# Kernel optimization log

Hardware: AMD Instinct MI355X
Metric: run time of the kernel (lower is better)

## Reference

```python
import jax, jax.numpy as jnp
import numpy as np

TEMPERATURE = 0.5
NEG_FILL = -9000000000000000.0


def setup_inputs() -> dict:
    key = jax.random.key(0)
    k1, k2 = jax.random.split(key)
    z1 = jax.random.normal(k1, (4096, 256), dtype=jnp.float32)
    z2 = jax.random.normal(k2, (4096, 256), dtype=jnp.float32)
    return {"z1": z1, "z2": z2}


def reference(z1, z2):
    N = z1.shape[0]
    z = jnp.concatenate([z1, z2], axis=0)  # [2N, d]
    # cosine similarity: normalize once (eps matches torch's 1e-8) then GEMM
    norm = jnp.maximum(jnp.linalg.norm(z, axis=-1, keepdims=True), 1e-8)
    zn = z / norm
    sim = (zn @ zn.T) / TEMPERATURE  # [2N, 2N]
    # mask out self-similarity on the diagonal
    diag = jnp.eye(2 * N, dtype=bool)
    sim = jnp.where(diag, NEG_FILL, sim)
    labels = jnp.concatenate([jnp.arange(N) + N, jnp.arange(N)])  # positive pairs
    logp = jax.nn.log_softmax(sim, axis=-1)
    loss = -jnp.mean(jnp.take_along_axis(logp, labels[:, None], axis=1))
    return loss
```

## Files before the change

kernel.cpp:

```cpp
#include <hip/hip_runtime.h>
#include <hip/hip_bf16.h>


#define TWO_N 8192
#define NPAIR 4096
#define DDIM  256
#define NT    64
#define NBLK  (NT * (NT + 1) / 2)
#define INV_T 2.0f
#define GEMM_GRID 256

typedef __attribute__((ext_vector_type(8))) short bf16x8;
typedef __attribute__((ext_vector_type(4))) float f32x4;

typedef __attribute__((address_space(1))) void gvoid_t;
typedef __attribute__((address_space(3))) void lvoid_t;

__device__ __forceinline__ void gload_lds16(const void* g, void* l) {
    __builtin_amdgcn_global_load_lds((gvoid_t*)g, (lvoid_t*)l, 16, 0, 0);
}

__global__ void k_normalize(const float* __restrict__ z1,
                            const float* __restrict__ z2,
                            __hip_bfloat16* __restrict__ zn,
                            float* __restrict__ e_diag,
                            float* __restrict__ pos,
                            float* __restrict__ row_sumexp,
                            float* __restrict__ out) {
    if (threadIdx.x < 8) row_sumexp[blockIdx.x * 8 + threadIdx.x] = 0.0f;
    if (blockIdx.x == 0 && threadIdx.x == 0) out[0] = 0.0f;

    const int w    = threadIdx.x >> 6;
    const int lane = threadIdx.x & 63;
    const int i    = blockIdx.x * 4 + w;

    float4 a = ((const float4*)(z1 + (size_t)i * DDIM))[lane];
    float4 b = ((const float4*)(z2 + (size_t)i * DDIM))[lane];

    float s1 = a.x * a.x + a.y * a.y + a.z * a.z + a.w * a.w;
    float s2 = b.x * b.x + b.y * b.y + b.z * b.z + b.w * b.w;
    float dd = a.x * b.x + a.y * b.y + a.z * b.z + a.w * b.w;
#pragma unroll
    for (int m = 1; m < 64; m <<= 1) {
        s1 += __shfl_xor(s1, m, 64);
        s2 += __shfl_xor(s2, m, 64);
        dd += __shfl_xor(dd, m, 64);
    }

    float inv1 = 1.0f / fmaxf(sqrtf(s1), 1e-8f);
    float inv2 = 1.0f / fmaxf(sqrtf(s2), 1e-8f);

    __hip_bfloat16 q1[4], q2[4];
    q1[0] = __float2bfloat16(a.x * inv1); q1[1] = __float2bfloat16(a.y * inv1);
    q1[2] = __float2bfloat16(a.z * inv1); q1[3] = __float2bfloat16(a.w * inv1);
    q2[0] = __float2bfloat16(b.x * inv2); q2[1] = __float2bfloat16(b.y * inv2);
    q2[2] = __float2bfloat16(b.z * inv2); q2[3] = __float2bfloat16(b.w * inv2);

    float qs1 = 0.0f, qs2 = 0.0f;
#pragma unroll
    for (int j = 0; j < 4; ++j) {
        float f1 = __bfloat162float(q1[j]);
        float f2 = __bfloat162float(q2[j]);
        qs1 += f1 * f1;
        qs2 += f2 * f2;
    }
#pragma unroll
    for (int m = 1; m < 64; m <<= 1) {
        qs1 += __shfl_xor(qs1, m, 64);
        qs2 += __shfl_xor(qs2, m, 64);
    }

    *reinterpret_cast<uint2*>(zn + (size_t)i * DDIM + lane * 4) =
        *reinterpret_cast<uint2*>(q1);
    *reinterpret_cast<uint2*>(zn + (size_t)(i + NPAIR) * DDIM + lane * 4) =
        *reinterpret_cast<uint2*>(q2);

    if (lane == 0) {
        e_diag[i]         = __expf(qs1 * INV_T);
        e_diag[i + NPAIR] = __expf(qs2 * INV_T);
        pos[i]            = dd * inv1 * inv2 * INV_T;
    }
}

__global__ __launch_bounds__(512, 2)
void k_gemm_sumexp(const __hip_bfloat16* __restrict__ zn,
                   float* __restrict__ row_sumexp) {
    __shared__ __align__(128) __hip_bfloat16 Asmem[128 * DDIM];

    const int tid  = threadIdx.x;
    const int lane = tid & 63;
    const int w    = tid >> 6;
    const int wr   = w >> 2;
    const int wc   = w & 3;
    const int lr   = lane & 15;
    const int quad = lane >> 4;

    const int t0 = (blockIdx.x * NBLK) >> 8;
    const int t1 = ((blockIdx.x + 1) * NBLK) >> 8;

    int b = t0;
    int rt = (int)(64.5f - sqrtf(64.5f * 64.5f - 2.0f * (float)b));
    if (rt < 0) rt = 0;
    if (rt > NT - 1) rt = NT - 1;
    while (rt > 0 && NT * rt - (rt * (rt - 1)) / 2 > b) --rt;
    while (NT * (rt + 1) - ((rt + 1) * rt) / 2 <= b) ++rt;
    int ct = rt + (b - (NT * rt - (rt * (rt - 1)) / 2));

    int cur_rt = -1;
    f32x4 acc[4][2];
    int  pRow = 0, pCol = 0;
    bool pDiag = false, havePrev = false;

    auto epilogue = [&]() {
        float rs[4][4], cs[2];
#pragma unroll
        for (int mi = 0; mi < 4; ++mi)
#pragma unroll
            for (int r = 0; r < 4; ++r) rs[mi][r] = 0.0f;
        cs[0] = cs[1] = 0.0f;
#pragma unroll
        for (int mi = 0; mi < 4; ++mi)
#pragma unroll
            for (int ni = 0; ni < 2; ++ni)
#pragma unroll
                for (int r = 0; r < 4; ++r) {
                    float e = __expf(acc[mi][ni][r] * INV_T);
                    rs[mi][r] += e;
                    cs[ni] += e;
                }
#pragma unroll
        for (int mi = 0; mi < 4; ++mi)
#pragma unroll
            for (int r = 0; r < 4; ++r) {
                float v = rs[mi][r];
                v += __shfl_xor(v, 1, 64);
                v += __shfl_xor(v, 2, 64);
                v += __shfl_xor(v, 4, 64);
                v += __shfl_xor(v, 8, 64);
                if (lr == 0)
                    atomicAdd(&row_sumexp[pRow + wr * 64 + mi * 16 + quad * 4 + r], v);
            }
        if (!pDiag) {
#pragma unroll
            for (int ni = 0; ni < 2; ++ni) {
                float v = cs[ni];
                v += __shfl_xor(v, 16, 64);
                v += __shfl_xor(v, 32, 64);
                if (quad == 0)
                    atomicAdd(&row_sumexp[pCol + wc * 32 + ni * 16 + lr], v);
            }
        }
    };

    for (int t = t0; t < t1; ++t) {
        const int  row_base = rt * 128;
        const int  col_base = ct * 128;
        const bool diag     = (rt == ct);
        const bool restage  = (rt != cur_rt);

        if (restage) {
            __syncthreads();
            const int ck = (tid & 24) | ((tid & 7) ^ ((tid >> 5) & 7));
            const char* gA = (const char*)(zn + (size_t)row_base * DDIM)
                           + (tid >> 5) * (DDIM * 2) + ck * 16;
            char* lA = (char*)Asmem + tid * 16;
#pragma unroll
            for (int j = 0; j < 8; ++j)
                gload_lds16(gA + (size_t)j * 16 * (DDIM * 2), lA + j * 8192);
            cur_rt = rt;
        }

        const __hip_bfloat16* gB0 =
            zn + (size_t)(col_base + wc * 32 + lr) * DDIM + quad * 8;
        bf16x8 Bfr[8][2];
#pragma unroll
        for (int ks = 0; ks < 8; ++ks) {
            const __hip_bfloat16* p0 = gB0 + ks * 32;
            const __hip_bfloat16* p1 = p0 + 16 * DDIM;
            asm volatile("global_load_dwordx4 %0, %1, off"
                         : "=v"(Bfr[ks][0]) : "v"(p0) : "memory");
            asm volatile("global_load_dwordx4 %0, %1, off"
                         : "=v"(Bfr[ks][1]) : "v"(p1) : "memory");
        }

        if (havePrev) epilogue();
        havePrev = true; pRow = row_base; pCol = col_base; pDiag = diag;

        int pa[4];
#pragma unroll
        for (int mi = 0; mi < 4; ++mi)
            pa[mi] = (wr * 64 + mi * 16 + lr) * (DDIM * 2) + ((quad ^ (lr & 7)) << 4);

        bf16x8 afc[4];
        if (restage) {
            asm volatile("s_waitcnt vmcnt(0)" ::: "memory");
            __syncthreads();
#pragma unroll
            for (int mi = 0; mi < 4; ++mi)
                afc[mi] = *(const bf16x8*)((const char*)Asmem + pa[mi]);
        } else {
#pragma unroll
            for (int mi = 0; mi < 4; ++mi)
                afc[mi] = *(const bf16x8*)((const char*)Asmem + pa[mi]);
            asm volatile("s_waitcnt vmcnt(16)" ::: "memory");
        }
        __builtin_amdgcn_sched_barrier(0);

#pragma unroll
        for (int mi = 0; mi < 4; ++mi)
#pragma unroll
            for (int ni = 0; ni < 2; ++ni)
                acc[mi][ni] = (f32x4){0.f, 0.f, 0.f, 0.f};

#pragma unroll
        for (int kstep = 0; kstep < 8; ++kstep) {
            bf16x8 afn[4];
            if (kstep < 7) {
                const int kn   = kstep + 1;
                const int koff = (kn >> 1) << 7;
                const int kx   = (kn & 1) << 6;
#pragma unroll
                for (int mi = 0; mi < 4; ++mi)
                    afn[mi] = *(const bf16x8*)((const char*)Asmem + ((pa[mi] ^ kx) + koff));
            }
#pragma unroll
            for (int mi = 0; mi < 4; ++mi)
#pragma unroll
                for (int ni = 0; ni < 2; ++ni)
                    acc[mi][ni] = __builtin_amdgcn_mfma_f32_16x16x32_bf16(
                        afc[mi], Bfr[kstep][ni], acc[mi][ni], 0, 0, 0);
            if (kstep < 7) {
#pragma unroll
                for (int mi = 0; mi < 4; ++mi) afc[mi] = afn[mi];
            }
        }

        if (++ct >= NT) { ++rt; ct = rt; }
    }

    epilogue();
}

__global__ void k_final(const float* __restrict__ row_sumexp,
                        const float* __restrict__ e_diag,
                        const float* __restrict__ pos,
                        float* __restrict__ out) {
    const int i    = blockIdx.x * 256 + threadIdx.x;
    const int w    = threadIdx.x >> 6;
    const int lane = threadIdx.x & 63;

    float t = logf(row_sumexp[i] - e_diag[i])
            + logf(row_sumexp[i + NPAIR] - e_diag[i + NPAIR])
            - 2.0f * pos[i];
#pragma unroll
    for (int m = 1; m < 64; m <<= 1) t += __shfl_xor(t, m, 64);

    __shared__ float ps[4];
    if (lane == 0) ps[w] = t;
    __syncthreads();
    if (threadIdx.x == 0) {
        float s = (ps[0] + ps[1] + ps[2] + ps[3]) * (1.0f / (float)TWO_N);
        atomicAdd(out, s);
    }
}

extern "C" void kernel_launch(void* const* d_in, const int* in_sizes, int n_in,
                              void* d_out, int out_size, void* d_ws, size_t ws_size,
                              hipStream_t stream) {
    const float* z1 = (const float*)d_in[0];
    const float* z2 = (const float*)d_in[1];
    float* out = (float*)d_out;

    char* ws = (char*)d_ws;
    __hip_bfloat16* zn  = (__hip_bfloat16*)ws;
    float* row_sumexp   = (float*)(ws + (size_t)TWO_N * DDIM * 2);
    float* e_diag       = row_sumexp + TWO_N;
    float* pos          = e_diag + TWO_N;

    k_normalize<<<NPAIR / 4, 256, 0, stream>>>(z1, z2, zn, e_diag, pos,
                                               row_sumexp, out);
    k_gemm_sumexp<<<GEMM_GRID, 512, 0, stream>>>(zn, row_sumexp);
    k_final<<<NPAIR / 256, 256, 0, stream>>>(row_sumexp, e_diag, pos, out);
}
```

Baseline: 128.6 us.

## Double GEMM grid, keep row sums in registers, split B loads around epilogue

Doubles the GEMM grid so each block handles about half as many triangular tiles. Row partial sums now stay in registers across all tiles that share a row tile, and the atomics are flushed only when the row tile changes, which cuts row atomics. B-fragment loads are split into two halves around the exp-accumulate epilogue so more of the global load latency is hidden. The risks are extra register pressure from the persistent row sums, and the `vmcnt(2)` wait, which lets the last B loads still be in flight when the first k-steps run.

```diff
diff --git a/kernel.cpp b/kernel.cpp
--- a/kernel.cpp
+++ b/kernel.cpp
@@ -8,7 +8,7 @@
 #define NT    64
 #define NBLK  (NT * (NT + 1) / 2)
 #define INV_T 2.0f
-#define GEMM_GRID 256
+#define GEMM_GRID 512
 
 typedef __attribute__((ext_vector_type(8))) short bf16x8;
 typedef __attribute__((ext_vector_type(4))) float f32x4;
@@ -95,8 +95,8 @@
     const int lr   = lane & 15;
     const int quad = lane >> 4;
 
-    const int t0 = (blockIdx.x * NBLK) >> 8;
-    const int t1 = ((blockIdx.x + 1) * NBLK) >> 8;
+    const int t0 = (int)(((long)blockIdx.x * NBLK) >> 9);
+    const int t1 = (int)(((long)(blockIdx.x + 1) * NBLK) >> 9);
 
     int b = t0;
     int rt = (int)(64.5f - sqrtf(64.5f * 64.5f - 2.0f * (float)b));
@@ -106,28 +106,43 @@
     while (NT * (rt + 1) - ((rt + 1) * rt) / 2 <= b) ++rt;
     int ct = rt + (b - (NT * rt - (rt * (rt - 1)) / 2));
 
+    int pa[4];
+#pragma unroll
+    for (int mi = 0; mi < 4; ++mi)
+        pa[mi] = (wr * 64 + mi * 16 + lr) * (DDIM * 2) + ((quad ^ (lr & 7)) << 4);
+
     int cur_rt = -1;
     f32x4 acc[4][2];
-    int  pRow = 0, pCol = 0;
+    float rs[4][4];
+#pragma unroll
+    for (int mi = 0; mi < 4; ++mi)
+#pragma unroll
+        for (int r = 0; r < 4; ++r) rs[mi][r] = 0.0f;
+    int  pCol = 0;
     bool pDiag = false, havePrev = false;
 
-    auto epilogue = [&]() {
-        float rs[4][4], cs[2];
+    auto epi_accum = [&](float& cs0, float& cs1) {
 #pragma unroll
         for (int mi = 0; mi < 4; ++mi)
 #pragma unroll
-            for (int r = 0; r < 4; ++r) rs[mi][r] = 0.0f;
-        cs[0] = cs[1] = 0.0f;
-#pragma unroll
-        for (int mi = 0; mi < 4; ++mi)
-#pragma unroll
-            for (int ni = 0; ni < 2; ++ni)
-#pragma unroll
-                for (int r = 0; r < 4; ++r) {
-                    float e = __expf(acc[mi][ni][r] * INV_T);
-                    rs[mi][r] += e;
-                    cs[ni] += e;
-                }
+            for (int r = 0; r < 4; ++r) {
+                float e0 = __expf(acc[mi][0][r] * INV_T);
+                float e1 = __expf(acc[mi][1][r] * INV_T);
+                rs[mi][r] += e0 + e1;
+                cs0 += e0;
+                cs1 += e1;
+            }
+    };
+    auto epi_cols = [&](float cs0, float cs1) {
+        if (pDiag) { cs0 = 0.0f; cs1 = 0.0f; }
+        cs0 += __shfl_xor(cs0, 16, 64); cs0 += __shfl_xor(cs0, 32, 64);
+        cs1 += __shfl_xor(cs1, 16, 64); cs1 += __shfl_xor(cs1, 32, 64);
+        if (quad == 0) {
+            atomicAdd(&row_sumexp[pCol + wc * 32 + lr], cs0);
+            atomicAdd(&row_sumexp[pCol + wc * 32 + 16 + lr], cs1);
+        }
+    };
+    auto flush_rows = [&](int rowb) {
 #pragma unroll
         for (int mi = 0; mi < 4; ++mi)
 #pragma unroll
@@ -138,18 +153,9 @@
                 v += __shfl_xor(v, 4, 64);
                 v += __shfl_xor(v, 8, 64);
                 if (lr == 0)
-                    atomicAdd(&row_sumexp[pRow + wr * 64 + mi * 16 + quad * 4 + r], v);
-            }
-        if (!pDiag) {
-#pragma unroll
-            for (int ni = 0; ni < 2; ++ni) {
-                float v = cs[ni];
-                v += __shfl_xor(v, 16, 64);
-                v += __shfl_xor(v, 32, 64);
-                if (quad == 0)
-                    atomicAdd(&row_sumexp[pCol + wc * 32 + ni * 16 + lr], v);
-            }
-        }
+                    atomicAdd(&row_sumexp[rowb + wr * 64 + mi * 16 + quad * 4 + r], v);
+                rs[mi][r] = 0.0f;
+            }
     };
 
     for (int t = t0; t < t1; ++t) {
@@ -158,7 +164,13 @@
         const bool diag     = (rt == ct);
         const bool restage  = (rt != cur_rt);
 
+        const __hip_bfloat16* gB0 =
+            zn + (size_t)(col_base + wc * 32 + lr) * DDIM + quad * 8;
+        bf16x8 Bfr[8][2];
+
         if (restage) {
+            if (havePrev) { float c0 = 0.f, c1 = 0.f; epi_accum(c0, c1); epi_cols(c0, c1); }
+            if (cur_rt >= 0) flush_rows(cur_rt * 128);
             __syncthreads();
             const int ck = (tid & 24) | ((tid & 7) ^ ((tid >> 5) & 7));
             const char* gA = (const char*)(zn + (size_t)row_base * DDIM)
@@ -167,50 +179,56 @@
 #pragma unroll
             for (int j = 0; j < 8; ++j)
                 gload_lds16(gA + (size_t)j * 16 * (DDIM * 2), lA + j * 8192);
+#pragma unroll
+            for (int ks = 0; ks < 8; ++ks) {
+                const __hip_bfloat16* p0 = gB0 + ks * 32;
+                const __hip_bfloat16* p1 = p0 + 16 * DDIM;
+                asm volatile("global_load_dwordx4 %0, %1, off"
+                             : "=v"(Bfr[ks][0]) : "v"(p0) : "memory");
+                asm volatile("global_load_dwordx4 %0, %1, off"
+                             : "=v"(Bfr[ks][1]) : "v"(p1) : "memory");
+            }
             cur_rt = rt;
-        }
-
-        const __hip_bfloat16* gB0 =
-            zn + (size_t)(col_base + wc * 32 + lr) * DDIM + quad * 8;
-        bf16x8 Bfr[8][2];
-#pragma unroll
-        for (int ks = 0; ks < 8; ++ks) {
-            const __hip_bfloat16* p0 = gB0 + ks * 32;
-            const __hip_bfloat16* p1 = p0 + 16 * DDIM;
-            asm volatile("global_load_dwordx4 %0, %1, off"
-                         : "=v"(Bfr[ks][0]) : "v"(p0) : "memory");
-            asm volatile("global_load_dwordx4 %0, %1, off"
-                         : "=v"(Bfr[ks][1]) : "v"(p1) : "memory");
-        }
-
-        if (havePrev) epilogue();
-        havePrev = true; pRow = row_base; pCol = col_base; pDiag = diag;
-
-        int pa[4];
-#pragma unroll
-        for (int mi = 0; mi < 4; ++mi)
-            pa[mi] = (wr * 64 + mi * 16 + lr) * (DDIM * 2) + ((quad ^ (lr & 7)) << 4);
-
-        bf16x8 afc[4];
-        if (restage) {
             asm volatile("s_waitcnt vmcnt(0)" ::: "memory");
             __syncthreads();
-#pragma unroll
-            for (int mi = 0; mi < 4; ++mi)
-                afc[mi] = *(const bf16x8*)((const char*)Asmem + pa[mi]);
         } else {
 #pragma unroll
-            for (int mi = 0; mi < 4; ++mi)
-                afc[mi] = *(const bf16x8*)((const char*)Asmem + pa[mi]);
-            asm volatile("s_waitcnt vmcnt(16)" ::: "memory");
+            for (int ks = 0; ks < 4; ++ks) {
+                const __hip_bfloat16* p0 = gB0 + ks * 32;
+                const __hip_bfloat16* p1 = p0 + 16 * DDIM;
+                asm volatile("global_load_dwordx4 %0, %1, off"
+                             : "=v"(Bfr[ks][0]) : "v"(p0) : "memory");
+                asm volatile("global_load_dwordx4 %0, %1, off"
+                             : "=v"(Bfr[ks][1]) : "v"(p1) : "memory");
+            }
+            float c0 = 0.f, c1 = 0.f;
+            epi_accum(c0, c1);
+#pragma unroll
+            for (int ks = 4; ks < 8; ++ks) {
+                const __hip_bfloat16* p0 = gB0 + ks * 32;
+                const __hip_bfloat16* p1 = p0 + 16 * DDIM;
+                asm volatile("global_load_dwordx4 %0, %1, off"
+                             : "=v"(Bfr[ks][0]) : "v"(p0) : "memory");
+                asm volatile("global_load_dwordx4 %0, %1, off"
+                             : "=v"(Bfr[ks][1]) : "v"(p1) : "memory");
+            }
+            epi_cols(c0, c1);
+            asm volatile("s_waitcnt vmcnt(2)" ::: "memory");
         }
         __builtin_amdgcn_sched_barrier(0);
 
+        pCol = col_base; pDiag = diag; havePrev = true;
+
 #pragma unroll
         for (int mi = 0; mi < 4; ++mi)
 #pragma unroll
             for (int ni = 0; ni < 2; ++ni)
                 acc[mi][ni] = (f32x4){0.f, 0.f, 0.f, 0.f};
+
+        bf16x8 afc[4];
+#pragma unroll
+        for (int mi = 0; mi < 4; ++mi)
+            afc[mi] = *(const bf16x8*)((const char*)Asmem + pa[mi]);
 
 #pragma unroll
         for (int kstep = 0; kstep < 8; ++kstep) {
@@ -238,7 +256,8 @@
         if (++ct >= NT) { ++rt; ct = rt; }
     }
 
-    epilogue();
+    { float c0 = 0.f, c1 = 0.f; epi_accum(c0, c1); epi_cols(c0, c1); }
+    flush_rows(cur_rt * 128);
 }
 
 __global__ void k_final(const float* __restrict__ row_sumexp,
```

Result: slower. 132.0 us (+2.6%).

## Replace symmetric triangular tiling with full row-panel GEMM and row-only sumexp

Applied to the files above, without the earlier changes.

Each block now owns one 128-row panel and an eighth of the columns, computing the full similarity matrix rather than only the upper triangle. Row sums accumulate in registers across tiles, with one set of atomics at the end and no column-sum atomics. This removes the triangular index setup, panel restaging and column atomic traffic. The cost is roughly double the matrix-multiply and exp work, plus a full memory wait each tile instead of a partial one.

```diff
diff --git a/kernel.cpp b/kernel.cpp
--- a/kernel.cpp
+++ b/kernel.cpp
@@ -6,9 +6,7 @@
 #define NPAIR 4096
 #define DDIM  256
 #define NT    64
-#define NBLK  (NT * (NT + 1) / 2)
 #define INV_T 2.0f
-#define GEMM_GRID 256
 
 typedef __attribute__((ext_vector_type(8))) short bf16x8;
 typedef __attribute__((ext_vector_type(4))) float f32x4;
@@ -83,8 +81,8 @@
 }
 
 __global__ __launch_bounds__(512, 2)
-void k_gemm_sumexp(const __hip_bfloat16* __restrict__ zn,
-                   float* __restrict__ row_sumexp) {
+void k_gemm_rows(const __hip_bfloat16* __restrict__ zn,
+                 float* __restrict__ row_sumexp) {
     __shared__ __align__(128) __hip_bfloat16 Asmem[128 * DDIM];
 
     const int tid  = threadIdx.x;
@@ -95,83 +93,48 @@
     const int lr   = lane & 15;
     const int quad = lane >> 4;
 
-    const int t0 = (blockIdx.x * NBLK) >> 8;
-    const int t1 = ((blockIdx.x + 1) * NBLK) >> 8;
-
-    int b = t0;
-    int rt = (int)(64.5f - sqrtf(64.5f * 64.5f - 2.0f * (float)b));
-    if (rt < 0) rt = 0;
-    if (rt > NT - 1) rt = NT - 1;
-    while (rt > 0 && NT * rt - (rt * (rt - 1)) / 2 > b) --rt;
-    while (NT * (rt + 1) - ((rt + 1) * rt) / 2 <= b) ++rt;
-    int ct = rt + (b - (NT * rt - (rt * (rt - 1)) / 2));
-
-    int cur_rt = -1;
+    const int panel    = blockIdx.x >> 3;
+    const int chunk    = blockIdx.x & 7;
+    const int row_base = panel * 128;
+
+    {
+        const int ck = (tid & 24) | ((tid & 7) ^ ((tid >> 5) & 7));
+        const char* gA = (const char*)(zn + (size_t)row_base * DDIM)
+                       + (tid >> 5) * (DDIM * 2) + ck * 16;
+        char* lA = (char*)Asmem + tid * 16;
+#pragma unroll
+        for (int j = 0; j < 8; ++j)
+            gload_lds16(gA + (size_t)j * 16 * (DDIM * 2), lA + j * 8192);
+    }
+
+    int pa[4];
+#pragma unroll
+    for (int mi = 0; mi < 4; ++mi)
+        pa[mi] = (wr * 64 + mi * 16 + lr) * (DDIM * 2) + ((quad ^ (lr & 7)) << 4);
+
     f32x4 acc[4][2];
-    int  pRow = 0, pCol = 0;
-    bool pDiag = false, havePrev = false;
-
-    auto epilogue = [&]() {
-        float rs[4][4], cs[2];
+    float rs[4][4];
+#pragma unroll
+    for (int mi = 0; mi < 4; ++mi)
+#pragma unroll
+        for (int r = 0; r < 4; ++r) rs[mi][r] = 0.0f;
+
+    auto epi_accum = [&]() {
 #pragma unroll
         for (int mi = 0; mi < 4; ++mi)
 #pragma unroll
-            for (int r = 0; r < 4; ++r) rs[mi][r] = 0.0f;
-        cs[0] = cs[1] = 0.0f;
-#pragma unroll
-        for (int mi = 0; mi < 4; ++mi)
-#pragma unroll
-            for (int ni = 0; ni < 2; ++ni)
-#pragma unroll
-                for (int r = 0; r < 4; ++r) {
-                    float e = __expf(acc[mi][ni][r] * INV_T);
-                    rs[mi][r] += e;
-                    cs[ni] += e;
-                }
-#pragma unroll
-        for (int mi = 0; mi < 4; ++mi)
-#pragma unroll
             for (int r = 0; r < 4; ++r) {
-                float v = rs[mi][r];
-                v += __shfl_xor(v, 1, 64);
-                v += __shfl_xor(v, 2, 64);
-                v += __shfl_xor(v, 4, 64);
-                v += __shfl_xor(v, 8, 64);
-                if (lr == 0)
-                    atomicAdd(&row_sumexp[pRow + wr * 64 + mi * 16 + quad * 4 + r], v);
+                rs[mi][r] += __expf(acc[mi][0][r] * INV_T)
+                           + __expf(acc[mi][1][r] * INV_T);
             }
-        if (!pDiag) {
-#pragma unroll
-            for (int ni = 0; ni < 2; ++ni) {
-                float v = cs[ni];
-                v += __shfl_xor(v, 16, 64);
-                v += __shfl_xor(v, 32, 64);
-                if (quad == 0)
-                    atomicAdd(&row_sumexp[pCol + wc * 32 + ni * 16 + lr], v);
-            }
-        }
     };
 
-    for (int t = t0; t < t1; ++t) {
-        const int  row_base = rt * 128;
-        const int  col_base = ct * 128;
-        const bool diag     = (rt == ct);
-        const bool restage  = (rt != cur_rt);
-
-        if (restage) {
-            __syncthreads();
-            const int ck = (tid & 24) | ((tid & 7) ^ ((tid >> 5) & 7));
-            const char* gA = (const char*)(zn + (size_t)row_base * DDIM)
-                           + (tid >> 5) * (DDIM * 2) + ck * 16;
-            char* lA = (char*)Asmem + tid * 16;
-#pragma unroll
-            for (int j = 0; j < 8; ++j)
-                gload_lds16(gA + (size_t)j * 16 * (DDIM * 2), lA + j * 8192);
-            cur_rt = rt;
-        }
-
+#pragma unroll 1
+    for (int tt = 0; tt < 8; ++tt) {
+        const int col_base = (chunk * 8 + tt) * 128;
         const __hip_bfloat16* gB0 =
             zn + (size_t)(col_base + wc * 32 + lr) * DDIM + quad * 8;
+
         bf16x8 Bfr[8][2];
 #pragma unroll
         for (int ks = 0; ks < 8; ++ks) {
@@ -183,26 +146,12 @@
                          : "=v"(Bfr[ks][1]) : "v"(p1) : "memory");
         }
 
-        if (havePrev) epilogue();
-        havePrev = true; pRow = row_base; pCol = col_base; pDiag = diag;
-
-        int pa[4];
-#pragma unroll
-        for (int mi = 0; mi < 4; ++mi)
-            pa[mi] = (wr * 64 + mi * 16 + lr) * (DDIM * 2) + ((quad ^ (lr & 7)) << 4);
-
-        bf16x8 afc[4];
-        if (restage) {
+        if (tt == 0) {
             asm volatile("s_waitcnt vmcnt(0)" ::: "memory");
             __syncthreads();
-#pragma unroll
-            for (int mi = 0; mi < 4; ++mi)
-                afc[mi] = *(const bf16x8*)((const char*)Asmem + pa[mi]);
         } else {
-#pragma unroll
-            for (int mi = 0; mi < 4; ++mi)
-                afc[mi] = *(const bf16x8*)((const char*)Asmem + pa[mi]);
-            asm volatile("s_waitcnt vmcnt(16)" ::: "memory");
+            epi_accum();
+            asm volatile("s_waitcnt vmcnt(0)" ::: "memory");
         }
         __builtin_amdgcn_sched_barrier(0);
 
@@ -211,6 +160,11 @@
 #pragma unroll
             for (int ni = 0; ni < 2; ++ni)
                 acc[mi][ni] = (f32x4){0.f, 0.f, 0.f, 0.f};
+
+        bf16x8 afc[4];
+#pragma unroll
+        for (int mi = 0; mi < 4; ++mi)
+            afc[mi] = *(const bf16x8*)((const char*)Asmem + pa[mi]);
 
 #pragma unroll
         for (int kstep = 0; kstep < 8; ++kstep) {
@@ -234,11 +188,23 @@
                 for (int mi = 0; mi < 4; ++mi) afc[mi] = afn[mi];
             }
         }
-
-        if (++ct >= NT) { ++rt; ct = rt; }
-    }
-
-    epilogue();
+    }
+
+    epi_accum();
+
+#pragma unroll
+    for (int mi = 0; mi < 4; ++mi) {
+#pragma unroll
+        for (int r = 0; r < 4; ++r) {
+            float v = rs[mi][r];
+            v += __shfl_xor(v, 1, 64);
+            v += __shfl_xor(v, 2, 64);
+            v += __shfl_xor(v, 4, 64);
+            v += __shfl_xor(v, 8, 64);
+            if (lr == 0)
+                atomicAdd(&row_sumexp[row_base + wr * 64 + mi * 16 + quad * 4 + r], v);
+        }
+    }
 }
 
 __global__ void k_final(const float* __restrict__ row_sumexp,
@@ -279,6 +245,6 @@
 
     k_normalize<<<NPAIR / 4, 256, 0, stream>>>(z1, z2, zn, e_diag, pos,
                                                row_sumexp, out);
-    k_gemm_sumexp<<<GEMM_GRID, 512, 0, stream>>>(zn, row_sumexp);
+    k_gemm_rows<<<NT * 8, 512, 0, stream>>>(zn, row_sumexp);
     k_final<<<NPAIR / 256, 256, 0, stream>>>(row_sumexp, e_diag, pos, out);
 }
```

Result: slower. 132.9 us (+3.3%).
